# Optimization experiments

Measured on AMD Instinct MI355X. Metric: run time of the kernel, lower is better.

## Reference

```python
import jax, jax.numpy as jnp
import numpy as np

LB_WEIGHT = 0.01  # load_balance_loss_weight


def setup_inputs() -> dict:
    key = jax.random.key(0)
    ks = jax.random.split(key, 5)
    B, S, D, F, E = 2, 2048, 1024, 4096, 8
    scale = 0.02
    return {
        "x": jax.random.normal(ks[0], (B, S, D), dtype=jnp.float32),
        "Wr": jax.random.normal(ks[1], (E, D), dtype=jnp.float32) * scale,
        "W1": jax.random.normal(ks[2], (E, F, D), dtype=jnp.float32) * scale,
        "b1": jnp.zeros((E, F), dtype=jnp.float32),
        "W2": jax.random.normal(ks[3], (E, D, F), dtype=jnp.float32) * scale,
        "b2": jnp.zeros((E, D), dtype=jnp.float32),
        "top_k": 2,
    }


def reference(x, Wr, W1, b1, W2, b2, top_k):
    B, S, D = x.shape
    E = Wr.shape[0]
    x_flat = x.reshape(-1, D)                      # (T, D)

    # Router: softmax over experts, then top-k with renormalized gates.
    router_logits = x_flat @ Wr.T                  # (T, E)
    router_probs = jax.nn.softmax(router_logits, axis=-1)
    topk_p, topk_idx = jax.lax.top_k(router_probs, top_k)   # (T, K)
    topk_p = topk_p / jnp.sum(topk_p, axis=-1, keepdims=True)

    # Combine weights per expert: w[t, e] = sum_k topk_p[t, k] * [idx[t, k] == e]
    one_hot = jax.nn.one_hot(topk_idx, E, dtype=x.dtype)     # (T, K, E)
    combine = jnp.einsum("tk,tke->te", topk_p, one_hot)      # (T, E)

    # Expert FFNs (dense over all experts; masked-out experts get zero weight).
    # FeedForward: Linear(D->F) -> GELU -> Linear(F->D); dropout is identity (eval).
    h = jnp.einsum("td,efd->tef", x_flat, W1) + b1           # (T, E, F)
    h = jax.nn.gelu(h)
    expert_out = jnp.einsum("tef,edf->ted", h, W2) + b2      # (T, E, D)

    out_flat = jnp.einsum("te,ted->td", combine, expert_out) # (T, D)
    output = out_flat.reshape(B, S, D)

    # Load-balance aux loss.
    expert_usage = jnp.mean(router_probs, axis=0)            # (E,)
    aux_loss = LB_WEIGHT * jnp.sum((expert_usage - 1.0 / E) ** 2)
    return output, aux_loss
```

## Files before the change

### kernel.cpp

```cpp
#include <hip/hip_runtime.h>
#include <hip/hip_bf16.h>
#include <stdint.h>

#define D_DIM 1024
#define F_DIM 4096
#define E_NUM 8
#define BM 128
#define BN 128
#define BK 64
#define MAXTILES 72

typedef __attribute__((ext_vector_type(4))) float f32x4;
typedef __attribute__((ext_vector_type(8))) short bf16x8;

#define C_CNT   0
#define C_CUR   8
#define C_OFF   16
#define C_NT    25
#define C_TE    26
#define C_TR    (26+MAXTILES)
#define C_USAGE (26+2*MAXTILES)

__device__ __forceinline__ void gload_lds16(const void* g, void* l) {
  __builtin_amdgcn_global_load_lds((const __attribute__((address_space(1))) void*)g,
                                   (__attribute__((address_space(3))) void*)l, 16, 0, 0);
}

__device__ __forceinline__ float bf2f(unsigned short u) {
  union { unsigned int i; float f; } c; c.i = ((unsigned int)u) << 16; return c.f;
}

__global__ void cvt_k(const float* __restrict__ s, unsigned short* __restrict__ d, int n4) {
  const int stride = gridDim.x * blockDim.x;
  for (int i = blockIdx.x * blockDim.x + threadIdx.x; i < n4; i += stride) {
    float4 v = ((const float4*)s)[i];
    __hip_bfloat16 h0 = __float2bfloat16(v.x);
    __hip_bfloat16 h1 = __float2bfloat16(v.y);
    __hip_bfloat16 h2 = __float2bfloat16(v.z);
    __hip_bfloat16 h3 = __float2bfloat16(v.w);
    ushort4 o;
    o.x = *(unsigned short*)&h0; o.y = *(unsigned short*)&h1;
    o.z = *(unsigned short*)&h2; o.w = *(unsigned short*)&h3;
    ((ushort4*)d)[i] = o;
  }
}

__global__ __launch_bounds__(256) void router_k(
    const float* __restrict__ x, const float* __restrict__ Wr,
    int* __restrict__ t2i, float* __restrict__ t2g,
    float* __restrict__ usage_part, unsigned short* __restrict__ xb, int T) {
  __shared__ float us[4][E_NUM];
  const int wave = threadIdx.x >> 6;
  const int lane = threadIdx.x & 63;
  const int gw = blockIdx.x * 4 + wave;
  const float4* xt = (const float4*)(x + (size_t)gw * D_DIM);
  const float4* wr4 = (const float4*)Wr;
  unsigned short* xrow = xb + (size_t)gw * D_DIM;
  float l[E_NUM] = {0.f,0.f,0.f,0.f,0.f,0.f,0.f,0.f};
#pragma unroll
  for (int it = 0; it < D_DIM / 256; it++) {
    const int i4 = it * 64 + lane;
    const float4 xv = xt[i4];
    __hip_bfloat16 c0 = __float2bfloat16(xv.x), c1 = __float2bfloat16(xv.y);
    __hip_bfloat16 c2 = __float2bfloat16(xv.z), c3 = __float2bfloat16(xv.w);
    ushort4 ov; ov.x = *(unsigned short*)&c0; ov.y = *(unsigned short*)&c1;
    ov.z = *(unsigned short*)&c2; ov.w = *(unsigned short*)&c3;
    ((ushort4*)xrow)[i4] = ov;
#pragma unroll
    for (int e = 0; e < E_NUM; e++) {
      const float4 w = wr4[e * (D_DIM / 4) + i4];
      l[e] += xv.x * w.x + xv.y * w.y + xv.z * w.z + xv.w * w.w;
    }
  }
#pragma unroll
  for (int e = 0; e < E_NUM; e++) {
    float v = l[e];
    v += __shfl_xor(v, 32); v += __shfl_xor(v, 16); v += __shfl_xor(v, 8);
    v += __shfl_xor(v, 4);  v += __shfl_xor(v, 2);  v += __shfl_xor(v, 1);
    l[e] = v;
  }
  float m = l[0];
#pragma unroll
  for (int e = 1; e < E_NUM; e++) m = fmaxf(m, l[e]);
  float p[E_NUM]; float s = 0.f;
#pragma unroll
  for (int e = 0; e < E_NUM; e++) { p[e] = expf(l[e] - m); s += p[e]; }
  const float inv = 1.0f / s;
  float v1 = l[0]; int i1 = 0;
#pragma unroll
  for (int e = 1; e < E_NUM; e++) { if (l[e] > v1) { v1 = l[e]; i1 = e; } }
  float v2 = -3.0e38f; int i2 = 0;
#pragma unroll
  for (int e = 0; e < E_NUM; e++) { if (e != i1 && l[e] > v2) { v2 = l[e]; i2 = e; } }
  const float p1 = expf(v1 - m);
  const float p2 = expf(v2 - m);
  const float gd = 1.0f / (p1 + p2);
  if (lane == 0) {
    t2i[gw * 2] = i1; t2i[gw * 2 + 1] = i2;
    t2g[gw * 2] = p1 * gd; t2g[gw * 2 + 1] = p2 * gd;
#pragma unroll
    for (int e = 0; e < E_NUM; e++) us[wave][e] = p[e] * inv;
  }
  __syncthreads();
  if (threadIdx.x < E_NUM) {
    const int e = threadIdx.x;
    usage_part[blockIdx.x * E_NUM + e] = us[0][e] + us[1][e] + us[2][e] + us[3][e];
  }
}

__global__ __launch_bounds__(256) void reduce_k(
    const float* __restrict__ usage_part, const int* __restrict__ t2i,
    int* __restrict__ ctrl, int nblk, int T2) {
  __shared__ float usum[E_NUM];
  __shared__ int hist[E_NUM];
  if (threadIdx.x < E_NUM) { usum[threadIdx.x] = 0.f; hist[threadIdx.x] = 0; }
  __syncthreads();
  {
    const int e = threadIdx.x & 7;
    const int chunk = threadIdx.x >> 3;
    float s = 0.f;
    for (int i = chunk; i < nblk; i += 32) s += usage_part[i * E_NUM + e];
    atomicAdd(&usum[e], s);
  }
  {
    int h[E_NUM] = {0,0,0,0,0,0,0,0};
    for (int i = threadIdx.x; i < T2; i += 256) h[t2i[i] & 7]++;
#pragma unroll
    for (int e = 0; e < E_NUM; e++) if (h[e]) atomicAdd(&hist[e], h[e]);
  }
  __syncthreads();
  if (threadIdx.x < E_NUM) {
    ctrl[C_CNT + threadIdx.x] = hist[threadIdx.x];
    ((float*)(ctrl + C_USAGE))[threadIdx.x] = usum[threadIdx.x];
  }
}

__global__ void offsets_k(int* __restrict__ ctrl, float* __restrict__ aux_out, int T) {
  if (threadIdx.x == 0) {
    int off = 0, nt = 0;
    for (int e = 0; e < E_NUM; e++) {
      ctrl[C_OFF + e] = off;
      ctrl[C_CUR + e] = off;
      const int c = ctrl[C_CNT + e];
      const int ntile = (c + BM - 1) / BM;
      for (int i = 0; i < ntile; i++) {
        ctrl[C_TE + nt] = e;
        ctrl[C_TR + nt] = off + i * BM;
        nt++;
      }
      off += c;
    }
    ctrl[C_OFF + E_NUM] = off;
    ctrl[C_NT] = nt;
    const float* usage = (const float*)(ctrl + C_USAGE);
    float loss = 0.f;
    for (int e = 0; e < E_NUM; e++) {
      const float um = usage[e] / (float)T - 1.0f / (float)E_NUM;
      loss += um * um;
    }
    aux_out[0] = 0.01f * loss;
  }
}

__global__ void scatter_k(const int* __restrict__ t2i, int* __restrict__ ctrl,
                          int* __restrict__ rmap, int* __restrict__ slots, int T) {
  const int t = blockIdx.x * blockDim.x + threadIdx.x;
  if (t >= T) return;
#pragma unroll
  for (int k = 0; k < 2; k++) {
    const int e = t2i[t * 2 + k];
    const int slot = atomicAdd(&ctrl[C_CUR + e], 1);
    rmap[slot] = t;
    slots[t * 2 + k] = slot;
  }
}

__global__ __launch_bounds__(256) void gemm1_k(
    const unsigned short* __restrict__ xb, const unsigned short* __restrict__ W1b,
    const float* __restrict__ b1, unsigned short* __restrict__ hb,
    const int* __restrict__ rmap, const int* __restrict__ ctrl, int T2) {
  __shared__ __align__(16) unsigned short As[2][BM * BK];
  __shared__ __align__(16) unsigned short Bs[2][BN * BK];
  const int lin = blockIdx.x;
  const int lin2 = (lin & 7) * 288 + (lin >> 3);
  const int tile = lin2 >> 5;
  const int fbase = (lin2 & 31) * BN;

  const int nt = ctrl[C_NT];
  if (tile >= nt) return;
  const int e = ctrl[C_TE + tile];
  const int rowbase = ctrl[C_TR + tile];
  const int row_end = ctrl[C_OFF + e + 1];

  const int tid = threadIdx.x;
  const int lane = tid & 63;
  const int wave = tid >> 6;

  const unsigned short* a_src[4];
  const unsigned short* b_src[4];
  char* aL0[4]; char* bL0[4]; char* aL1[4]; char* bL1[4];
#pragma unroll
  for (int i = 0; i < 4; i++) {
    const int c = tid + 256 * i;
    const int r = c >> 3, cc = c & 7;
    const int sc = cc ^ (r & 7);
    int pos = rowbase + r; pos = pos < T2 ? pos : T2 - 1;
    a_src[i] = xb + (size_t)rmap[pos] * D_DIM + sc * 8;
    b_src[i] = W1b + ((size_t)e * F_DIM + (size_t)(fbase + r)) * D_DIM + sc * 8;
    aL0[i] = (char*)As[0] + (wave * 64 + 256 * i) * 16;
    bL0[i] = (char*)Bs[0] + (wave * 64 + 256 * i) * 16;
    aL1[i] = (char*)As[1] + (wave * 64 + 256 * i) * 16;
    bL1[i] = (char*)Bs[1] + (wave * 64 + 256 * i) * 16;
  }

  f32x4 acc[4][4] = {};
  const int wm = wave >> 1, wn = wave & 1;
  const int rA = wm * 64 + (lane & 15);
  const int rB = wn * 64 + (lane & 15);
  const int swz = lane & 7;
  const int ckq = lane >> 4;

#define STAGE1(K0, AL, BL)                                         \
  {                                                                \
    _Pragma("unroll")                                              \
    for (int i = 0; i < 4; i++) gload_lds16(a_src[i] + (K0), AL[i]); \
    _Pragma("unroll")                                              \
    for (int i = 0; i < 4; i++) gload_lds16(b_src[i] + (K0), BL[i]); \
  }

#define COMPUTE1(AC, BC)                                            \
  {                                                                 \
    _Pragma("unroll")                                               \
    for (int kh = 0; kh < 2; ++kh) {                                \
      const int co = (((kh * 4 + ckq) ^ swz) << 4);                 \
      bf16x8 af[4], bfv[4];                                         \
      _Pragma("unroll")                                             \
      for (int mi = 0; mi < 4; mi++)                                \
        af[mi] = *(const bf16x8*)((const char*)(AC) + (rA + mi * 16) * 128 + co); \
      _Pragma("unroll")                                             \
      for (int ni = 0; ni < 4; ni++)                                \
        bfv[ni] = *(const bf16x8*)((const char*)(BC) + (rB + ni * 16) * 128 + co); \
      _Pragma("unroll")                                             \
      for (int mi = 0; mi < 4; mi++)                                \
        _Pragma("unroll")                                           \
        for (int ni = 0; ni < 4; ni++)                              \
          acc[mi][ni] = __builtin_amdgcn_mfma_f32_16x16x32_bf16(af[mi], bfv[ni], acc[mi][ni], 0, 0, 0); \
    }                                                               \
  }

  STAGE1(0, aL0, bL0);
  const int NK = D_DIM / BK;
  for (int kt = 0; kt < NK; kt += 2) {
    STAGE1((kt + 1) * BK, aL1, bL1);
    asm volatile("s_waitcnt vmcnt(8)" ::: "memory");
    __builtin_amdgcn_s_barrier();
    __builtin_amdgcn_sched_barrier(0);
    COMPUTE1(As[0], Bs[0]);
    __builtin_amdgcn_sched_barrier(0);
    __builtin_amdgcn_s_barrier();
    if (kt + 2 < NK) {
      STAGE1((kt + 2) * BK, aL0, bL0);
      asm volatile("s_waitcnt vmcnt(8)" ::: "memory");
    } else {
      asm volatile("s_waitcnt vmcnt(0)" ::: "memory");
    }
    __builtin_amdgcn_s_barrier();
    __builtin_amdgcn_sched_barrier(0);
    COMPUTE1(As[1], Bs[1]);
    __builtin_amdgcn_sched_barrier(0);
    __builtin_amdgcn_s_barrier();
  }
#undef STAGE1
#undef COMPUTE1

  const int r_rem = row_end - rowbase;
  const float* b1e = b1 + (size_t)e * F_DIM;
#pragma unroll
  for (int mi = 0; mi < 4; mi++) {
#pragma unroll
    for (int ni = 0; ni < 4; ni++) {
      const int col = fbase + wn * 64 + ni * 16 + (lane & 15);
      const float bias = b1e[col];
#pragma unroll
      for (int q = 0; q < 4; q++) {
        const int rr = wm * 64 + mi * 16 + (lane >> 4) * 4 + q;
        if (rr < r_rem) {
          const float v = acc[mi][ni][q] + bias;
          const float u2 = 1.5957691216057308f * (v + 0.044715f * v * v * v);
          const float gg = v / (1.0f + __expf(-u2));
          __hip_bfloat16 hv = __float2bfloat16(gg);
          hb[(size_t)(rowbase + rr) * F_DIM + col] = *(unsigned short*)&hv;
        }
      }
    }
  }
}

__global__ __launch_bounds__(256) void gemm2_k(
    const unsigned short* __restrict__ hb, const unsigned short* __restrict__ W2b,
    unsigned short* __restrict__ y2, const int* __restrict__ ctrl, int T2) {
  __shared__ __align__(16) unsigned short As[2][BM * BK];
  __shared__ __align__(16) unsigned short Bs[2][BN * BK];
  const int lin = blockIdx.x;
  const int lin2 = (lin & 7) * 144 + (lin >> 3);
  const int tile = lin2 >> 4;
  const int rr2 = lin2 & 15;
  const int z = rr2 >> 3;
  const int dbase = (rr2 & 7) * BN;

  const int nt = ctrl[C_NT];
  if (tile >= nt) return;
  const int e = ctrl[C_TE + tile];
  const int rowbase = ctrl[C_TR + tile];
  const int row_end = ctrl[C_OFF + e + 1];
  const int kt0 = z * (F_DIM / BK / 2);

  const int tid = threadIdx.x;
  const int lane = tid & 63;
  const int wave = tid >> 6;

  const unsigned short* a_src[4];
  const unsigned short* b_src[4];
  char* aL0[4]; char* bL0[4]; char* aL1[4]; char* bL1[4];
#pragma unroll
  for (int i = 0; i < 4; i++) {
    const int c = tid + 256 * i;
    const int r = c >> 3, cc = c & 7;
    const int sc = cc ^ (r & 7);
    int pos = rowbase + r; pos = pos < T2 ? pos : T2 - 1;
    a_src[i] = hb + (size_t)pos * F_DIM + sc * 8;
    b_src[i] = W2b + ((size_t)e * D_DIM + (size_t)(dbase + r)) * F_DIM + sc * 8;
    aL0[i] = (char*)As[0] + (wave * 64 + 256 * i) * 16;
    bL0[i] = (char*)Bs[0] + (wave * 64 + 256 * i) * 16;
    aL1[i] = (char*)As[1] + (wave * 64 + 256 * i) * 16;
    bL1[i] = (char*)Bs[1] + (wave * 64 + 256 * i) * 16;
  }

  f32x4 acc[4][4] = {};
  const int wm = wave >> 1, wn = wave & 1;
  const int rA = wm * 64 + (lane & 15);
  const int rB = wn * 64 + (lane & 15);
  const int swz = lane & 7;
  const int ckq = lane >> 4;

#define STAGE2(K0, AL, BL)                                         \
  {                                                                \
    _Pragma("unroll")                                              \
    for (int i = 0; i < 4; i++) gload_lds16(a_src[i] + (K0), AL[i]); \
    _Pragma("unroll")                                              \
    for (int i = 0; i < 4; i++) gload_lds16(b_src[i] + (K0), BL[i]); \
  }

#define COMPUTE2(AC, BC)                                            \
  {                                                                 \
    _Pragma("unroll")                                               \
    for (int kh = 0; kh < 2; ++kh) {                                \
      const int co = (((kh * 4 + ckq) ^ swz) << 4);                 \
      bf16x8 af[4], bfv[4];                                         \
      _Pragma("unroll")                                             \
      for (int mi = 0; mi < 4; mi++)                                \
        af[mi] = *(const bf16x8*)((const char*)(AC) + (rA + mi * 16) * 128 + co); \
      _Pragma("unroll")                                             \
      for (int ni = 0; ni < 4; ni++)                                \
        bfv[ni] = *(const bf16x8*)((const char*)(BC) + (rB + ni * 16) * 128 + co); \
      _Pragma("unroll")                                             \
      for (int mi = 0; mi < 4; mi++)                                \
        _Pragma("unroll")                                           \
        for (int ni = 0; ni < 4; ni++)                              \
          acc[mi][ni] = __builtin_amdgcn_mfma_f32_16x16x32_bf16(af[mi], bfv[ni], acc[mi][ni], 0, 0, 0); \
    }                                                               \
  }

  const int NKH = F_DIM / BK / 2;
  STAGE2(kt0 * BK, aL0, bL0);
  for (int kt = kt0; kt < kt0 + NKH; kt += 2) {
    STAGE2((kt + 1) * BK, aL1, bL1);
    asm volatile("s_waitcnt vmcnt(8)" ::: "memory");
    __builtin_amdgcn_s_barrier();
    __builtin_amdgcn_sched_barrier(0);
    COMPUTE2(As[0], Bs[0]);
    __builtin_amdgcn_sched_barrier(0);
    __builtin_amdgcn_s_barrier();
    if (kt + 2 < kt0 + NKH) {
      STAGE2((kt + 2) * BK, aL0, bL0);
      asm volatile("s_waitcnt vmcnt(8)" ::: "memory");
    } else {
      asm volatile("s_waitcnt vmcnt(0)" ::: "memory");
    }
    __builtin_amdgcn_s_barrier();
    __builtin_amdgcn_sched_barrier(0);
    COMPUTE2(As[1], Bs[1]);
    __builtin_amdgcn_sched_barrier(0);
    __builtin_amdgcn_s_barrier();
  }
#undef STAGE2
#undef COMPUTE2

  const int r_rem = row_end - rowbase;
  unsigned short* yz = y2 + (size_t)z * T2 * D_DIM;
#pragma unroll
  for (int mi = 0; mi < 4; mi++) {
#pragma unroll
    for (int q = 0; q < 4; q++) {
      const int rr = wm * 64 + mi * 16 + (lane >> 4) * 4 + q;
      if (rr < r_rem) {
        const int pos = rowbase + rr;
#pragma unroll
        for (int ni = 0; ni < 4; ni++) {
          const int col = dbase + wn * 64 + ni * 16 + (lane & 15);
          __hip_bfloat16 hv = __float2bfloat16(acc[mi][ni][q]);
          yz[(size_t)pos * D_DIM + col] = *(unsigned short*)&hv;
        }
      }
    }
  }
}

__global__ __launch_bounds__(256) void combine_k(
    const unsigned short* __restrict__ y2, const float* __restrict__ b2,
    const int* __restrict__ t2i, const float* __restrict__ t2g,
    const int* __restrict__ slots, float* __restrict__ out, int T2) {
  const int t = blockIdx.x;
  const int c4 = threadIdx.x;
  const int s0 = slots[t * 2], s1 = slots[t * 2 + 1];
  const int e0 = t2i[t * 2], e1 = t2i[t * 2 + 1];
  const float g0 = t2g[t * 2], g1 = t2g[t * 2 + 1];
  const size_t half = (size_t)T2 * D_DIM;
  ushort4 a0 = ((const ushort4*)(y2 + (size_t)s0 * D_DIM))[c4];
  ushort4 a1 = ((const ushort4*)(y2 + half + (size_t)s0 * D_DIM))[c4];
  ushort4 b0 = ((const ushort4*)(y2 + (size_t)s1 * D_DIM))[c4];
  ushort4 b1v = ((const ushort4*)(y2 + half + (size_t)s1 * D_DIM))[c4];
  float4 bb0 = ((const float4*)(b2 + (size_t)e0 * D_DIM))[c4];
  float4 bb1 = ((const float4*)(b2 + (size_t)e1 * D_DIM))[c4];
  float4 o;
  o.x = g0 * (bf2f(a0.x) + bf2f(a1.x) + bb0.x) + g1 * (bf2f(b0.x) + bf2f(b1v.x) + bb1.x);
  o.y = g0 * (bf2f(a0.y) + bf2f(a1.y) + bb0.y) + g1 * (bf2f(b0.y) + bf2f(b1v.y) + bb1.y);
  o.z = g0 * (bf2f(a0.z) + bf2f(a1.z) + bb0.z) + g1 * (bf2f(b0.z) + bf2f(b1v.z) + bb1.z);
  o.w = g0 * (bf2f(a0.w) + bf2f(a1.w) + bb0.w) + g1 * (bf2f(b0.w) + bf2f(b1v.w) + bb1.w);
  ((float4*)(out + (size_t)t * D_DIM))[c4] = o;
}

extern "C" void kernel_launch(void* const* d_in, const int* in_sizes, int n_in,
                              void* d_out, int out_size, void* d_ws, size_t ws_size,
                              hipStream_t stream) {
  const float* x  = (const float*)d_in[0];
  const float* Wr = (const float*)d_in[1];
  const float* W1 = (const float*)d_in[2];
  const float* b1 = (const float*)d_in[3];
  const float* W2 = (const float*)d_in[4];
  const float* b2 = (const float*)d_in[5];
  float* out = (float*)d_out;

  const int T = in_sizes[0] / D_DIM;
  const int T2 = T * 2;
  const int nblk = T / 4;

  char* ws = (char*)d_ws;
  size_t o = 0;
  unsigned short* xb  = (unsigned short*)(ws + o); o += (size_t)T * D_DIM * 2;
  unsigned short* W1b = (unsigned short*)(ws + o); o += (size_t)E_NUM * F_DIM * D_DIM * 2;
  unsigned short* W2b = (unsigned short*)(ws + o); o += (size_t)E_NUM * D_DIM * F_DIM * 2;
  unsigned short* hb  = (unsigned short*)(ws + o); o += (size_t)T2 * F_DIM * 2;
  int*   ctrl  = (int*)(ws + o);   o += 4096;
  int*   t2i   = (int*)(ws + o);   o += (size_t)T2 * 4;
  float* t2g   = (float*)(ws + o); o += (size_t)T2 * 4;
  int*   rmap  = (int*)(ws + o);   o += (size_t)T2 * 4;
  int*   slots = (int*)(ws + o);   o += (size_t)T2 * 4;
  float* usage_part = (float*)(ws + o); o += (size_t)nblk * E_NUM * 4;
  unsigned short* y2 = W1b;

  hipMemsetAsync(ctrl, 0, 4096, stream);

  cvt_k<<<1024, 256, 0, stream>>>(W1, W1b, E_NUM * F_DIM * D_DIM / 4);
  cvt_k<<<1024, 256, 0, stream>>>(W2, W2b, E_NUM * D_DIM * F_DIM / 4);

  router_k<<<nblk, 256, 0, stream>>>(x, Wr, t2i, t2g, usage_part, xb, T);
  reduce_k<<<1, 256, 0, stream>>>(usage_part, t2i, ctrl, nblk, T2);
  offsets_k<<<1, 64, 0, stream>>>(ctrl, out + (size_t)(out_size - 1), T);
  scatter_k<<<(T + 255) / 256, 256, 0, stream>>>(t2i, ctrl, rmap, slots, T);

  gemm1_k<<<MAXTILES * (F_DIM / BN), 256, 0, stream>>>(xb, W1b, b1, hb, rmap, ctrl, T2);
  gemm2_k<<<MAXTILES * (D_DIM / BN) * 2, 256, 0, stream>>>(hb, W2b, y2, ctrl, T2);
  combine_k<<<T, 256, 0, stream>>>(y2, b2, t2i, t2g, slots, out, T2);
}
```

Measured before the change: 418.3 us.

## Enlarge expert GEMM tiles to 256x256 with 512 threads and 4-way split-K

Both grouped expert GEMMs move from 128x128 tiles with 256 threads to 256x256 tiles with 512 threads. The double-buffered operands now live in 128KB of dynamic LDS, and each wave holds an 8x4 MFMA accumulator block. Routing offsets are padded to 256-row tiles, gemm2's split-K grows from 2 to 4 slices, and the combine kernel sums four partial outputs. The aim is more operand reuse per LDS byte and fewer global loads. The cost is lower occupancy (one large block per CU), more wasted padding rows per expert, and extra partial-sum traffic in combine.

```diff
diff --git a/kernel.cpp b/kernel.cpp
--- a/kernel.cpp
+++ b/kernel.cpp
@@ -5,10 +5,11 @@
 #define D_DIM 1024
 #define F_DIM 4096
 #define E_NUM 8
-#define BM 128
-#define BN 128
+#define BM2 256
+#define BN2 256
 #define BK 64
-#define MAXTILES 72
+#define MAXTILES 80
+#define MAXT256 40
 
 typedef __attribute__((ext_vector_type(4))) float f32x4;
 typedef __attribute__((ext_vector_type(8))) short bf16x8;
@@ -142,10 +143,10 @@
       ctrl[C_OFF + e] = off;
       ctrl[C_CUR + e] = off;
       const int c = ctrl[C_CNT + e];
-      const int ntile = (c + BM - 1) / BM;
+      const int ntile = (c + BM2 - 1) / BM2;
       for (int i = 0; i < ntile; i++) {
         ctrl[C_TE + nt] = e;
-        ctrl[C_TR + nt] = off + i * BM;
+        ctrl[C_TR + nt] = off + i * BM2;
         nt++;
       }
       off += c;
@@ -175,16 +176,43 @@
   }
 }
 
-__global__ __launch_bounds__(256) void gemm1_k(
+#define STAGE(K0, AL, BL)                                            \
+  {                                                                  \
+    _Pragma("unroll")                                                \
+    for (int i = 0; i < 4; i++) gload_lds16(a_src[i] + (K0), AL[i]); \
+    _Pragma("unroll")                                                \
+    for (int i = 0; i < 4; i++) gload_lds16(b_src[i] + (K0), BL[i]); \
+  }
+
+#define COMPUTE(AC, BC)                                              \
+  {                                                                  \
+    _Pragma("unroll")                                                \
+    for (int kh = 0; kh < 2; ++kh) {                                 \
+      const int co = (((kh * 4 + ckq) ^ swz) << 4);                  \
+      bf16x8 af[8], bfv[4];                                          \
+      _Pragma("unroll")                                              \
+      for (int mi = 0; mi < 8; mi++)                                 \
+        af[mi] = *(const bf16x8*)((AC) + (rA + mi * 16) * 128 + co); \
+      _Pragma("unroll")                                              \
+      for (int ni = 0; ni < 4; ni++)                                 \
+        bfv[ni] = *(const bf16x8*)((BC) + (rB + ni * 16) * 128 + co);\
+      _Pragma("unroll")                                              \
+      for (int mi = 0; mi < 8; mi++)                                 \
+        _Pragma("unroll")                                            \
+        for (int ni = 0; ni < 4; ni++)                               \
+          acc[mi][ni] = __builtin_amdgcn_mfma_f32_16x16x32_bf16(af[mi], bfv[ni], acc[mi][ni], 0, 0, 0); \
+    }                                                                \
+  }
+
+__global__ __launch_bounds__(512, 2) void gemm1_k(
     const unsigned short* __restrict__ xb, const unsigned short* __restrict__ W1b,
     const float* __restrict__ b1, unsigned short* __restrict__ hb,
     const int* __restrict__ rmap, const int* __restrict__ ctrl, int T2) {
-  __shared__ __align__(16) unsigned short As[2][BM * BK];
-  __shared__ __align__(16) unsigned short Bs[2][BN * BK];
+  extern __shared__ char smem[];
   const int lin = blockIdx.x;
-  const int lin2 = (lin & 7) * 288 + (lin >> 3);
-  const int tile = lin2 >> 5;
-  const int fbase = (lin2 & 31) * BN;
+  const int lin2 = (lin & 7) * 80 + (lin >> 3);
+  const int tile = lin2 >> 4;
+  const int fbase = (lin2 & 15) * BN2;
 
   const int nt = ctrl[C_NT];
   if (tile >= nt) return;
@@ -198,122 +226,96 @@
 
   const unsigned short* a_src[4];
   const unsigned short* b_src[4];
-  char* aL0[4]; char* bL0[4]; char* aL1[4]; char* bL1[4];
+  char *aL0[4], *bL0[4], *aL1[4], *bL1[4];
 #pragma unroll
   for (int i = 0; i < 4; i++) {
-    const int c = tid + 256 * i;
+    const int c = tid + 512 * i;
     const int r = c >> 3, cc = c & 7;
     const int sc = cc ^ (r & 7);
     int pos = rowbase + r; pos = pos < T2 ? pos : T2 - 1;
     a_src[i] = xb + (size_t)rmap[pos] * D_DIM + sc * 8;
     b_src[i] = W1b + ((size_t)e * F_DIM + (size_t)(fbase + r)) * D_DIM + sc * 8;
-    aL0[i] = (char*)As[0] + (wave * 64 + 256 * i) * 16;
-    bL0[i] = (char*)Bs[0] + (wave * 64 + 256 * i) * 16;
-    aL1[i] = (char*)As[1] + (wave * 64 + 256 * i) * 16;
-    bL1[i] = (char*)Bs[1] + (wave * 64 + 256 * i) * 16;
-  }
-
-  f32x4 acc[4][4] = {};
-  const int wm = wave >> 1, wn = wave & 1;
-  const int rA = wm * 64 + (lane & 15);
+    const int dst = wave * 1024 + i * 8192;
+    aL0[i] = smem + dst;          aL1[i] = smem + 32768 + dst;
+    bL0[i] = smem + 65536 + dst;  bL1[i] = smem + 98304 + dst;
+  }
+  const char* As0 = smem;          const char* As1 = smem + 32768;
+  const char* Bs0 = smem + 65536;  const char* Bs1 = smem + 98304;
+
+  f32x4 acc[8][4] = {};
+  const int wm = wave >> 2, wn = wave & 3;
+  const int rA = wm * 128 + (lane & 15);
   const int rB = wn * 64 + (lane & 15);
   const int swz = lane & 7;
   const int ckq = lane >> 4;
 
-#define STAGE1(K0, AL, BL)                                         \
-  {                                                                \
-    _Pragma("unroll")                                              \
-    for (int i = 0; i < 4; i++) gload_lds16(a_src[i] + (K0), AL[i]); \
-    _Pragma("unroll")                                              \
-    for (int i = 0; i < 4; i++) gload_lds16(b_src[i] + (K0), BL[i]); \
-  }
-
-#define COMPUTE1(AC, BC)                                            \
-  {                                                                 \
-    _Pragma("unroll")                                               \
-    for (int kh = 0; kh < 2; ++kh) {                                \
-      const int co = (((kh * 4 + ckq) ^ swz) << 4);                 \
-      bf16x8 af[4], bfv[4];                                         \
-      _Pragma("unroll")                                             \
-      for (int mi = 0; mi < 4; mi++)                                \
-        af[mi] = *(const bf16x8*)((const char*)(AC) + (rA + mi * 16) * 128 + co); \
-      _Pragma("unroll")                                             \
-      for (int ni = 0; ni < 4; ni++)                                \
-        bfv[ni] = *(const bf16x8*)((const char*)(BC) + (rB + ni * 16) * 128 + co); \
-      _Pragma("unroll")                                             \
-      for (int mi = 0; mi < 4; mi++)                                \
-        _Pragma("unroll")                                           \
-        for (int ni = 0; ni < 4; ni++)                              \
-          acc[mi][ni] = __builtin_amdgcn_mfma_f32_16x16x32_bf16(af[mi], bfv[ni], acc[mi][ni], 0, 0, 0); \
-    }                                                               \
-  }
-
-  STAGE1(0, aL0, bL0);
+  STAGE(0, aL0, bL0);
   const int NK = D_DIM / BK;
   for (int kt = 0; kt < NK; kt += 2) {
-    STAGE1((kt + 1) * BK, aL1, bL1);
+    STAGE((kt + 1) * BK, aL1, bL1);
     asm volatile("s_waitcnt vmcnt(8)" ::: "memory");
     __builtin_amdgcn_s_barrier();
     __builtin_amdgcn_sched_barrier(0);
-    COMPUTE1(As[0], Bs[0]);
+    COMPUTE(As0, Bs0);
     __builtin_amdgcn_sched_barrier(0);
     __builtin_amdgcn_s_barrier();
     if (kt + 2 < NK) {
-      STAGE1((kt + 2) * BK, aL0, bL0);
+      STAGE((kt + 2) * BK, aL0, bL0);
       asm volatile("s_waitcnt vmcnt(8)" ::: "memory");
     } else {
       asm volatile("s_waitcnt vmcnt(0)" ::: "memory");
     }
     __builtin_amdgcn_s_barrier();
     __builtin_amdgcn_sched_barrier(0);
-    COMPUTE1(As[1], Bs[1]);
-    __builtin_amdgcn_sched_barrier(0);
-    __builtin_amdgcn_s_barrier();
-  }
-#undef STAGE1
-#undef COMPUTE1
+    COMPUTE(As1, Bs1);
+    __builtin_amdgcn_sched_barrier(0);
+    __builtin_amdgcn_s_barrier();
+  }
 
   const int r_rem = row_end - rowbase;
   const float* b1e = b1 + (size_t)e * F_DIM;
-#pragma unroll
-  for (int mi = 0; mi < 4; mi++) {
-#pragma unroll
-    for (int ni = 0; ni < 4; ni++) {
-      const int col = fbase + wn * 64 + ni * 16 + (lane & 15);
-      const float bias = b1e[col];
-#pragma unroll
-      for (int q = 0; q < 4; q++) {
-        const int rr = wm * 64 + mi * 16 + (lane >> 4) * 4 + q;
-        if (rr < r_rem) {
-          const float v = acc[mi][ni][q] + bias;
+  float bias[4];
+#pragma unroll
+  for (int ni = 0; ni < 4; ni++)
+    bias[ni] = b1e[fbase + wn * 64 + ni * 16 + (lane & 15)];
+#pragma unroll
+  for (int mi = 0; mi < 8; mi++) {
+#pragma unroll
+    for (int q = 0; q < 4; q++) {
+      const int rr = wm * 128 + mi * 16 + (lane >> 4) * 4 + q;
+      if (rr < r_rem) {
+        unsigned short* hrow = hb + (size_t)(rowbase + rr) * F_DIM;
+#pragma unroll
+        for (int ni = 0; ni < 4; ni++) {
+          const int col = fbase + wn * 64 + ni * 16 + (lane & 15);
+          const float v = acc[mi][ni][q] + bias[ni];
           const float u2 = 1.5957691216057308f * (v + 0.044715f * v * v * v);
           const float gg = v / (1.0f + __expf(-u2));
           __hip_bfloat16 hv = __float2bfloat16(gg);
-          hb[(size_t)(rowbase + rr) * F_DIM + col] = *(unsigned short*)&hv;
+          hrow[col] = *(unsigned short*)&hv;
         }
       }
     }
   }
 }
 
-__global__ __launch_bounds__(256) void gemm2_k(
+__global__ __launch_bounds__(512, 2) void gemm2_k(
     const unsigned short* __restrict__ hb, const unsigned short* __restrict__ W2b,
     unsigned short* __restrict__ y2, const int* __restrict__ ctrl, int T2) {
-  __shared__ __align__(16) unsigned short As[2][BM * BK];
-  __shared__ __align__(16) unsigned short Bs[2][BN * BK];
+  extern __shared__ char smem[];
   const int lin = blockIdx.x;
-  const int lin2 = (lin & 7) * 144 + (lin >> 3);
+  const int lin2 = (lin & 7) * 80 + (lin >> 3);
   const int tile = lin2 >> 4;
-  const int rr2 = lin2 & 15;
-  const int z = rr2 >> 3;
-  const int dbase = (rr2 & 7) * BN;
+  const int rest = lin2 & 15;
+  const int z = rest >> 2;
+  const int dbase = (rest & 3) * BN2;
 
   const int nt = ctrl[C_NT];
   if (tile >= nt) return;
   const int e = ctrl[C_TE + tile];
   const int rowbase = ctrl[C_TR + tile];
   const int row_end = ctrl[C_OFF + e + 1];
-  const int kt0 = z * (F_DIM / BK / 2);
+  const int kt0 = z * (F_DIM / BK / 4);
 
   const int tid = threadIdx.x;
   const int lane = tid & 63;
@@ -321,95 +323,66 @@
 
   const unsigned short* a_src[4];
   const unsigned short* b_src[4];
-  char* aL0[4]; char* bL0[4]; char* aL1[4]; char* bL1[4];
+  char *aL0[4], *bL0[4], *aL1[4], *bL1[4];
 #pragma unroll
   for (int i = 0; i < 4; i++) {
-    const int c = tid + 256 * i;
+    const int c = tid + 512 * i;
     const int r = c >> 3, cc = c & 7;
     const int sc = cc ^ (r & 7);
     int pos = rowbase + r; pos = pos < T2 ? pos : T2 - 1;
     a_src[i] = hb + (size_t)pos * F_DIM + sc * 8;
     b_src[i] = W2b + ((size_t)e * D_DIM + (size_t)(dbase + r)) * F_DIM + sc * 8;
-    aL0[i] = (char*)As[0] + (wave * 64 + 256 * i) * 16;
-    bL0[i] = (char*)Bs[0] + (wave * 64 + 256 * i) * 16;
-    aL1[i] = (char*)As[1] + (wave * 64 + 256 * i) * 16;
-    bL1[i] = (char*)Bs[1] + (wave * 64 + 256 * i) * 16;
-  }
-
-  f32x4 acc[4][4] = {};
-  const int wm = wave >> 1, wn = wave & 1;
-  const int rA = wm * 64 + (lane & 15);
+    const int dst = wave * 1024 + i * 8192;
+    aL0[i] = smem + dst;          aL1[i] = smem + 32768 + dst;
+    bL0[i] = smem + 65536 + dst;  bL1[i] = smem + 98304 + dst;
+  }
+  const char* As0 = smem;          const char* As1 = smem + 32768;
+  const char* Bs0 = smem + 65536;  const char* Bs1 = smem + 98304;
+
+  f32x4 acc[8][4] = {};
+  const int wm = wave >> 2, wn = wave & 3;
+  const int rA = wm * 128 + (lane & 15);
   const int rB = wn * 64 + (lane & 15);
   const int swz = lane & 7;
   const int ckq = lane >> 4;
 
-#define STAGE2(K0, AL, BL)                                         \
-  {                                                                \
-    _Pragma("unroll")                                              \
-    for (int i = 0; i < 4; i++) gload_lds16(a_src[i] + (K0), AL[i]); \
-    _Pragma("unroll")                                              \
-    for (int i = 0; i < 4; i++) gload_lds16(b_src[i] + (K0), BL[i]); \
-  }
-
-#define COMPUTE2(AC, BC)                                            \
-  {                                                                 \
-    _Pragma("unroll")                                               \
-    for (int kh = 0; kh < 2; ++kh) {                                \
-      const int co = (((kh * 4 + ckq) ^ swz) << 4);                 \
-      bf16x8 af[4], bfv[4];                                         \
-      _Pragma("unroll")                                             \
-      for (int mi = 0; mi < 4; mi++)                                \
-        af[mi] = *(const bf16x8*)((const char*)(AC) + (rA + mi * 16) * 128 + co); \
-      _Pragma("unroll")                                             \
-      for (int ni = 0; ni < 4; ni++)                                \
-        bfv[ni] = *(const bf16x8*)((const char*)(BC) + (rB + ni * 16) * 128 + co); \
-      _Pragma("unroll")                                             \
-      for (int mi = 0; mi < 4; mi++)                                \
-        _Pragma("unroll")                                           \
-        for (int ni = 0; ni < 4; ni++)                              \
-          acc[mi][ni] = __builtin_amdgcn_mfma_f32_16x16x32_bf16(af[mi], bfv[ni], acc[mi][ni], 0, 0, 0); \
-    }                                                               \
-  }
-
-  const int NKH = F_DIM / BK / 2;
-  STAGE2(kt0 * BK, aL0, bL0);
+  const int NKH = F_DIM / BK / 4;
+  STAGE(kt0 * BK, aL0, bL0);
   for (int kt = kt0; kt < kt0 + NKH; kt += 2) {
-    STAGE2((kt + 1) * BK, aL1, bL1);
+    STAGE((kt + 1) * BK, aL1, bL1);
     asm volatile("s_waitcnt vmcnt(8)" ::: "memory");
     __builtin_amdgcn_s_barrier();
     __builtin_amdgcn_sched_barrier(0);
-    COMPUTE2(As[0], Bs[0]);
+    COMPUTE(As0, Bs0);
     __builtin_amdgcn_sched_barrier(0);
     __builtin_amdgcn_s_barrier();
     if (kt + 2 < kt0 + NKH) {
-      STAGE2((kt + 2) * BK, aL0, bL0);
+      STAGE((kt + 2) * BK, aL0, bL0);
       asm volatile("s_waitcnt vmcnt(8)" ::: "memory");
     } else {
       asm volatile("s_waitcnt vmcnt(0)" ::: "memory");
     }
     __builtin_amdgcn_s_barrier();
     __builtin_amdgcn_sched_barrier(0);
-    COMPUTE2(As[1], Bs[1]);
-    __builtin_amdgcn_sched_barrier(0);
-    __builtin_amdgcn_s_barrier();
-  }
-#undef STAGE2
-#undef COMPUTE2
+    COMPUTE(As1, Bs1);
+    __builtin_amdgcn_sched_barrier(0);
+    __builtin_amdgcn_s_barrier();
+  }
 
   const int r_rem = row_end - rowbase;
   unsigned short* yz = y2 + (size_t)z * T2 * D_DIM;
 #pragma unroll
-  for (int mi = 0; mi < 4; mi++) {
+  for (int mi = 0; mi < 8; mi++) {
 #pragma unroll
     for (int q = 0; q < 4; q++) {
-      const int rr = wm * 64 + mi * 16 + (lane >> 4) * 4 + q;
+      const int rr = wm * 128 + mi * 16 + (lane >> 4) * 4 + q;
       if (rr < r_rem) {
-        const int pos = rowbase + rr;
+        unsigned short* yrow = yz + (size_t)(rowbase + rr) * D_DIM;
 #pragma unroll
         for (int ni = 0; ni < 4; ni++) {
           const int col = dbase + wn * 64 + ni * 16 + (lane & 15);
           __hip_bfloat16 hv = __float2bfloat16(acc[mi][ni][q]);
-          yz[(size_t)pos * D_DIM + col] = *(unsigned short*)&hv;
+          yrow[col] = *(unsigned short*)&hv;
         }
       }
     }
@@ -425,18 +398,22 @@
   const int s0 = slots[t * 2], s1 = slots[t * 2 + 1];
   const int e0 = t2i[t * 2], e1 = t2i[t * 2 + 1];
   const float g0 = t2g[t * 2], g1 = t2g[t * 2 + 1];
-  const size_t half = (size_t)T2 * D_DIM;
-  ushort4 a0 = ((const ushort4*)(y2 + (size_t)s0 * D_DIM))[c4];
-  ushort4 a1 = ((const ushort4*)(y2 + half + (size_t)s0 * D_DIM))[c4];
-  ushort4 b0 = ((const ushort4*)(y2 + (size_t)s1 * D_DIM))[c4];
-  ushort4 b1v = ((const ushort4*)(y2 + half + (size_t)s1 * D_DIM))[c4];
+  const size_t sl = (size_t)T2 * D_DIM;
+  float sum0[4] = {0.f,0.f,0.f,0.f}, sum1[4] = {0.f,0.f,0.f,0.f};
+#pragma unroll
+  for (int zz = 0; zz < 4; zz++) {
+    ushort4 a = ((const ushort4*)(y2 + zz * sl + (size_t)s0 * D_DIM))[c4];
+    ushort4 b = ((const ushort4*)(y2 + zz * sl + (size_t)s1 * D_DIM))[c4];
+    sum0[0] += bf2f(a.x); sum0[1] += bf2f(a.y); sum0[2] += bf2f(a.z); sum0[3] += bf2f(a.w);
+    sum1[0] += bf2f(b.x); sum1[1] += bf2f(b.y); sum1[2] += bf2f(b.z); sum1[3] += bf2f(b.w);
+  }
   float4 bb0 = ((const float4*)(b2 + (size_t)e0 * D_DIM))[c4];
   float4 bb1 = ((const float4*)(b2 + (size_t)e1 * D_DIM))[c4];
   float4 o;
-  o.x = g0 * (bf2f(a0.x) + bf2f(a1.x) + bb0.x) + g1 * (bf2f(b0.x) + bf2f(b1v.x) + bb1.x);
-  o.y = g0 * (bf2f(a0.y) + bf2f(a1.y) + bb0.y) + g1 * (bf2f(b0.y) + bf2f(b1v.y) + bb1.y);
-  o.z = g0 * (bf2f(a0.z) + bf2f(a1.z) + bb0.z) + g1 * (bf2f(b0.z) + bf2f(b1v.z) + bb1.z);
-  o.w = g0 * (bf2f(a0.w) + bf2f(a1.w) + bb0.w) + g1 * (bf2f(b0.w) + bf2f(b1v.w) + bb1.w);
+  o.x = g0 * (sum0[0] + bb0.x) + g1 * (sum1[0] + bb1.x);
+  o.y = g0 * (sum0[1] + bb0.y) + g1 * (sum1[1] + bb1.y);
+  o.z = g0 * (sum0[2] + bb0.z) + g1 * (sum1[2] + bb1.z);
+  o.w = g0 * (sum0[3] + bb0.w) + g1 * (sum1[3] + bb1.w);
   ((float4*)(out + (size_t)t * D_DIM))[c4] = o;
 }
 
@@ -469,6 +446,9 @@
   float* usage_part = (float*)(ws + o); o += (size_t)nblk * E_NUM * 4;
   unsigned short* y2 = W1b;
 
+  hipFuncSetAttribute((const void*)gemm1_k, hipFuncAttributeMaxDynamicSharedMemorySize, 131072);
+  hipFuncSetAttribute((const void*)gemm2_k, hipFuncAttributeMaxDynamicSharedMemorySize, 131072);
+
   hipMemsetAsync(ctrl, 0, 4096, stream);
 
   cvt_k<<<1024, 256, 0, stream>>>(W1, W1b, E_NUM * F_DIM * D_DIM / 4);
@@ -479,7 +459,7 @@
   offsets_k<<<1, 64, 0, stream>>>(ctrl, out + (size_t)(out_size - 1), T);
   scatter_k<<<(T + 255) / 256, 256, 0, stream>>>(t2i, ctrl, rmap, slots, T);
 
-  gemm1_k<<<MAXTILES * (F_DIM / BN), 256, 0, stream>>>(xb, W1b, b1, hb, rmap, ctrl, T2);
-  gemm2_k<<<MAXTILES * (D_DIM / BN) * 2, 256, 0, stream>>>(hb, W2b, y2, ctrl, T2);
+  gemm1_k<<<MAXT256 * 16, 512, 131072, stream>>>(xb, W1b, b1, hb, rmap, ctrl, T2);
+  gemm2_k<<<MAXT256 * 16, 512, 131072, stream>>>(hb, W2b, y2, ctrl, T2);
   combine_k<<<T, 256, 0, stream>>>(y2, b2, t2i, t2g, slots, out, T2);
 }
```

Result: faster. 380.1 us, median of 2 (-9.1%).
